# Optimization experiments

Hardware: AMD Instinct MI355X
Metric: run time of the kernel (lower is better)

Reference implementation:

```python
import jax, jax.numpy as jnp
import numpy as np


def _mhc_kernels():
    # Malvar-He-Cutler 5x5 interpolation kernels, shape (4, 1, 5, 5) OIHW
    G_at_RB = np.array([[0, 0, -1, 0, 0], [0, 0, 2, 0, 0], [-1, 2, 4, 2, -1],
                        [0, 0, 2, 0, 0], [0, 0, -1, 0, 0]], dtype=np.float32) / 8
    R_at_G_Rrow = np.array([[0, 0, 0.5, 0, 0], [0, -1, 0, -1, 0], [-1, 4, 5, 4, -1],
                            [0, -1, 0, -1, 0], [0, 0, 0.5, 0, 0]], dtype=np.float32) / 8
    R_at_G_Brow = np.array([[0, 0, -1, 0, 0], [0, -1, 4, -1, 0], [0.5, 0, 5, 0, 0.5],
                            [0, -1, 4, -1, 0], [0, 0, -1, 0, 0]], dtype=np.float32) / 8
    R_at_B = np.array([[0, 0, -1.5, 0, 0], [0, 2, 0, 2, 0], [-1.5, 0, 6, 0, -1.5],
                       [0, 2, 0, 2, 0], [0, 0, -1.5, 0, 0]], dtype=np.float32) / 8
    return np.stack([G_at_RB, R_at_G_Rrow, R_at_G_Brow, R_at_B], axis=0)[:, None, :, :]


def setup_inputs() -> dict:
    key = jax.random.key(0)
    H, W = 4096, 6144  # 24 MP raw frame
    x = jax.random.randint(key, (H, W), 0, 16777216, dtype=jnp.int32)
    kernels = jnp.asarray(_mhc_kernels())  # fixed buffer values, (4,1,5,5)
    return {"x": x, "kernels": kernels}


def reference(x, kernels):
    xf = x.astype(jnp.float32)  # [H, W]
    # reflect pad by 2 and convolve with the 4 MHC kernels in one conv
    xp = jnp.pad(xf, 2, mode="reflect")[None, None]  # [1,1,H+4,W+4]
    res = jax.lax.conv_general_dilated(
        xp, kernels, window_strides=(1, 1), padding="VALID",
        dimension_numbers=("NCHW", "OIHW", "NCHW"))[0]  # [4, H, W]
    Gi, Rgr, Rgb, Rb = res[0], res[1], res[2], res[3]

    z = jnp.zeros_like(xf)
    # RGGB mosaic: R at (even,even), G at (even,odd)+(odd,even), B at (odd,odd)
    R = (z.at[::2, ::2].set(xf[::2, ::2])
           .at[::2, 1::2].set(Rgr[::2, 1::2])
           .at[1::2, ::2].set(Rgb[1::2, ::2])
           .at[1::2, 1::2].set(Rb[1::2, 1::2]))
    G = (z.at[::2, 1::2].set(xf[::2, 1::2])
           .at[1::2, ::2].set(xf[1::2, ::2])
           .at[::2, ::2].set(Gi[::2, ::2])
           .at[1::2, 1::2].set(Gi[1::2, 1::2]))
    B = (z.at[1::2, 1::2].set(xf[1::2, 1::2])
           .at[1::2, ::2].set(Rgr[1::2, ::2])
           .at[::2, 1::2].set(Rgb[::2, 1::2])
           .at[::2, ::2].set(Rb[::2, ::2]))

    rgb = jnp.stack([R, G, B], axis=-1)  # [H, W, 3]
    return jnp.clip(rgb, 0, 16777215).astype(jnp.int32)
```

## Files before the change

### kernel.cpp

```cpp
#include <hip/hip_runtime.h>

#define IMG_H 4096
#define IMG_W 6144

constexpr int TILE_W = 128;
constexpr int TILE_H = 16;
constexpr int LPAD   = 4;
constexpr int PITCH  = 136;
constexpr int LROWS  = 20;

typedef int i4 __attribute__((ext_vector_type(4)));

__device__ __forceinline__ int reflect_h(int r) {
    return r < 0 ? -r : (r >= IMG_H ? 2 * IMG_H - 2 - r : r);
}
__device__ __forceinline__ int reflect_w(int c) {
    return c < 0 ? -c : (c >= IMG_W ? 2 * IMG_W - 2 - c : c);
}
__device__ __forceinline__ int clampi(float v) {
    return (int)fminf(fmaxf(v, 0.f), 16777215.f);
}

__global__ __launch_bounds__(256)
void demosaic_kernel(const int* __restrict__ x, int* __restrict__ out) {
    __shared__ __align__(16) char smem[24576];
    float (*sin_)[PITCH] = (float (*)[PITCH])smem;
    int* sout = (int*)smem;

    const int tid = threadIdx.x;
    const int gx0 = blockIdx.x * TILE_W;
    const int gy0 = blockIdx.y * TILE_H;

    #pragma unroll
    for (int it = 0; it < 3; ++it) {
        int idx = tid + it * 256;
        if (idx < LROWS * 32) {
            int r = idx >> 5, v = idx & 31;
            int gr = reflect_h(gy0 + r - 2);
            i4 q = *(const i4*)(x + (long)gr * IMG_W + gx0 + 4 * v);
            float4 f = make_float4((float)q.x, (float)q.y, (float)q.z, (float)q.w);
            *(float4*)&sin_[r][LPAD + 4 * v] = f;
        }
    }
    if (tid < 80) {
        int r = tid >> 2, h = tid & 3;
        int gr = reflect_h(gy0 + r - 2);
        int lc = (h < 2) ? (2 + h) : (130 + h);
        int gc = reflect_w(gx0 + lc - LPAD);
        sin_[r][lc] = (float)x[(long)gr * IMG_W + gc];
    }
    __syncthreads();

    const int p  = tid & 63;
    const int ty = tid >> 6;
    const int cl = LPAD + 2 * p;

    int rr[4][6];

    #pragma unroll
    for (int k = 0; k < 4; ++k) {
        const int r = ty + 4 * k;
        float w[5][6];
        #pragma unroll
        for (int i = 0; i < 5; ++i) {
            float2 a  = *(const float2*)&sin_[r + i][cl - 2];
            float2 b  = *(const float2*)&sin_[r + i][cl];
            float2 c2 = *(const float2*)&sin_[r + i][cl + 2];
            w[i][0] = a.x;  w[i][1] = a.y;
            w[i][2] = b.x;  w[i][3] = b.y;
            w[i][4] = c2.x; w[i][5] = c2.y;
        }
        const float xe = w[2][2], xo = w[2][3];

        if ((ty & 1) == 0) {
            float Ge = (-w[0][2] + 2.f*(w[1][2]+w[3][2]) + 4.f*w[2][2] - w[4][2]
                        - w[2][0] + 2.f*(w[2][1]+w[2][3]) - w[2][4]) * 0.125f;
            float Ce = (-1.5f*(w[0][2]+w[4][2]+w[2][0]+w[2][4])
                        + 2.f*(w[1][1]+w[1][3]+w[3][1]+w[3][3]) + 6.f*w[2][2]) * 0.125f;
            float RRo = (0.5f*(w[0][3]+w[4][3]) - (w[1][2]+w[1][4]+w[3][2]+w[3][4])
                         - (w[2][1]+w[2][5]) + 4.f*(w[2][2]+w[2][4]) + 5.f*w[2][3]) * 0.125f;
            float RBo = (-(w[0][3]+w[4][3]) - (w[1][2]+w[1][4]+w[3][2]+w[3][4])
                         + 4.f*(w[1][3]+w[3][3]) + 0.5f*(w[2][1]+w[2][5]) + 5.f*w[2][3]) * 0.125f;
            rr[k][0] = clampi(xe);  rr[k][1] = clampi(Ge);  rr[k][2] = clampi(Ce);
            rr[k][3] = clampi(RRo); rr[k][4] = clampi(xo);  rr[k][5] = clampi(RBo);
        } else {
            float RBe = (-(w[0][2]+w[4][2]) - (w[1][1]+w[1][3]+w[3][1]+w[3][3])
                         + 4.f*(w[1][2]+w[3][2]) + 0.5f*(w[2][0]+w[2][4]) + 5.f*w[2][2]) * 0.125f;
            float RRe = (0.5f*(w[0][2]+w[4][2]) - (w[1][1]+w[1][3]+w[3][1]+w[3][3])
                         - (w[2][0]+w[2][4]) + 4.f*(w[2][1]+w[2][3]) + 5.f*w[2][2]) * 0.125f;
            float Co  = (-1.5f*(w[0][3]+w[4][3]+w[2][1]+w[2][5])
                         + 2.f*(w[1][2]+w[1][4]+w[3][2]+w[3][4]) + 6.f*w[2][3]) * 0.125f;
            float Go  = (-w[0][3] + 2.f*(w[1][3]+w[3][3]) + 4.f*w[2][3] - w[4][3]
                         - w[2][1] + 2.f*(w[2][2]+w[2][4]) - w[2][5]) * 0.125f;
            rr[k][0] = clampi(RBe); rr[k][1] = clampi(xe);  rr[k][2] = clampi(RRe);
            rr[k][3] = clampi(Co);  rr[k][4] = clampi(Go);  rr[k][5] = clampi(xo);
        }
    }

    __syncthreads();

    #pragma unroll
    for (int k = 0; k < 4; ++k) {
        int r = ty + 4 * k;
        int2* o = (int2*)&sout[r * (TILE_W * 3) + 6 * p];
        o[0] = make_int2(rr[k][0], rr[k][1]);
        o[1] = make_int2(rr[k][2], rr[k][3]);
        o[2] = make_int2(rr[k][4], rr[k][5]);
    }
    __syncthreads();

    #pragma unroll
    for (int it = 0; it < 6; ++it) {
        int j = tid + it * 256;
        i4 q = *(const i4*)&sout[4 * j];
        int r  = j / 96;
        int wv = j - r * 96;
        int* dst = out + (long)(gy0 + r) * (IMG_W * 3) + gx0 * 3 + 4 * wv;
        __builtin_nontemporal_store(q, (i4*)dst);
    }
}

extern "C" void kernel_launch(void* const* d_in, const int* in_sizes, int n_in,
                              void* d_out, int out_size, void* d_ws, size_t ws_size,
                              hipStream_t stream) {
    const int* x = (const int*)d_in[0];
    int* out = (int*)d_out;
    dim3 grid(IMG_W / TILE_W, IMG_H / TILE_H);
    demosaic_kernel<<<grid, 256, 0, stream>>>(x, out);
}
```

Baseline: 360.2 us.

## Replace LDS tiling with per-wave register sliding window over rows

```diff
diff --git a/kernel.cpp b/kernel.cpp
--- a/kernel.cpp
+++ b/kernel.cpp
@@ -3,76 +3,70 @@
 #define IMG_H 4096
 #define IMG_W 6144
 
-constexpr int TILE_W = 128;
-constexpr int TILE_H = 16;
-constexpr int LPAD   = 4;
-constexpr int PITCH  = 136;
-constexpr int LROWS  = 20;
+constexpr int SH  = 32;
+constexpr int NSX = IMG_W / 128;
+constexpr int NSY = IMG_H / SH;
 
-typedef int i4 __attribute__((ext_vector_type(4)));
+typedef int i2 __attribute__((ext_vector_type(2)));
 
 __device__ __forceinline__ int reflect_h(int r) {
     return r < 0 ? -r : (r >= IMG_H ? 2 * IMG_H - 2 - r : r);
-}
-__device__ __forceinline__ int reflect_w(int c) {
-    return c < 0 ? -c : (c >= IMG_W ? 2 * IMG_W - 2 - c : c);
 }
 __device__ __forceinline__ int clampi(float v) {
     return (int)fminf(fmaxf(v, 0.f), 16777215.f);
 }
 
+struct Row { i2 a, b, c; int fix; };
+
 __global__ __launch_bounds__(256)
-void demosaic_kernel(const int* __restrict__ x, int* __restrict__ out) {
-    __shared__ __align__(16) char smem[24576];
-    float (*sin_)[PITCH] = (float (*)[PITCH])smem;
-    int* sout = (int*)smem;
+void demosaic(const int* __restrict__ x, int* __restrict__ out) {
+    const int wid  = blockIdx.x * 4 + (threadIdx.x >> 6);
+    const int lane = threadIdx.x & 63;
+    const int sx = wid >> 7;
+    const int sy = wid & (NSY - 1);
+    const int gx0 = sx * 128;
+    const int gy0 = sy * SH;
+    const int ce  = gx0 + 2 * lane;
 
-    const int tid = threadIdx.x;
-    const int gx0 = blockIdx.x * TILE_W;
-    const int gy0 = blockIdx.y * TILE_H;
+    const int  cA = max(ce - 2, 0);
+    const int  cB = ce;
+    const int  cC = min(ce + 2, IMG_W - 2);
+    const bool pL = (ce == 0), pR = (ce == IMG_W - 2);
+    const bool pat = pL || pR;
+    const int  fixc = pL ? 2 : IMG_W - 3;
 
-    #pragma unroll
-    for (int it = 0; it < 3; ++it) {
-        int idx = tid + it * 256;
-        if (idx < LROWS * 32) {
-            int r = idx >> 5, v = idx & 31;
-            int gr = reflect_h(gy0 + r - 2);
-            i4 q = *(const i4*)(x + (long)gr * IMG_W + gx0 + 4 * v);
-            float4 f = make_float4((float)q.x, (float)q.y, (float)q.z, (float)q.w);
-            *(float4*)&sin_[r][LPAD + 4 * v] = f;
-        }
+    auto issue = [&](int y, Row& R) {
+        const int* rp = x + (long)reflect_h(y) * IMG_W;
+        R.a = *(const i2*)(rp + cA);
+        R.b = *(const i2*)(rp + cB);
+        R.c = *(const i2*)(rp + cC);
+        if (pat) R.fix = rp[fixc];
+    };
+    auto consume = [&](const Row& R, float* w6) {
+        w6[0] = (float)R.a.x; w6[1] = (float)R.a.y;
+        w6[2] = (float)R.b.x; w6[3] = (float)R.b.y;
+        w6[4] = (float)R.c.x; w6[5] = (float)R.c.y;
+        if (pat) { float f = (float)R.fix; if (pL) w6[0] = f; else w6[5] = f; }
+    };
+
+    float w[5][6];
+    {
+        Row t[4];
+        #pragma unroll
+        for (int i = 0; i < 4; ++i) issue(gy0 - 2 + i, t[i]);
+        #pragma unroll
+        for (int i = 0; i < 4; ++i) consume(t[i], w[i]);
     }
-    if (tid < 80) {
-        int r = tid >> 2, h = tid & 3;
-        int gr = reflect_h(gy0 + r - 2);
-        int lc = (h < 2) ? (2 + h) : (130 + h);
-        int gc = reflect_w(gx0 + lc - LPAD);
-        sin_[r][lc] = (float)x[(long)gr * IMG_W + gc];
-    }
-    __syncthreads();
+    Row pr[2];
+    issue(gy0 + 2, pr[0]);
+    issue(gy0 + 3, pr[1]);
 
-    const int p  = tid & 63;
-    const int ty = tid >> 6;
-    const int cl = LPAD + 2 * p;
+    int* op = out + (long)gy0 * (IMG_W * 3) + ce * 3;
 
-    int rr[4][6];
-
-    #pragma unroll
-    for (int k = 0; k < 4; ++k) {
-        const int r = ty + 4 * k;
-        float w[5][6];
-        #pragma unroll
-        for (int i = 0; i < 5; ++i) {
-            float2 a  = *(const float2*)&sin_[r + i][cl - 2];
-            float2 b  = *(const float2*)&sin_[r + i][cl];
-            float2 c2 = *(const float2*)&sin_[r + i][cl + 2];
-            w[i][0] = a.x;  w[i][1] = a.y;
-            w[i][2] = b.x;  w[i][3] = b.y;
-            w[i][4] = c2.x; w[i][5] = c2.y;
-        }
-        const float xe = w[2][2], xo = w[2][3];
-
-        if ((ty & 1) == 0) {
+    for (int i = 0; i < SH; i += 2) {
+        consume(pr[0], w[4]);
+        if (i < SH - 2) issue(gy0 + i + 4, pr[0]);
+        {
             float Ge = (-w[0][2] + 2.f*(w[1][2]+w[3][2]) + 4.f*w[2][2] - w[4][2]
                         - w[2][0] + 2.f*(w[2][1]+w[2][3]) - w[2][4]) * 0.125f;
             float Ce = (-1.5f*(w[0][2]+w[4][2]+w[2][0]+w[2][4])
@@ -81,9 +75,23 @@
                          - (w[2][1]+w[2][5]) + 4.f*(w[2][2]+w[2][4]) + 5.f*w[2][3]) * 0.125f;
             float RBo = (-(w[0][3]+w[4][3]) - (w[1][2]+w[1][4]+w[3][2]+w[3][4])
                          + 4.f*(w[1][3]+w[3][3]) + 0.5f*(w[2][1]+w[2][5]) + 5.f*w[2][3]) * 0.125f;
-            rr[k][0] = clampi(xe);  rr[k][1] = clampi(Ge);  rr[k][2] = clampi(Ce);
-            rr[k][3] = clampi(RRo); rr[k][4] = clampi(xo);  rr[k][5] = clampi(RBo);
-        } else {
+            i2 q0, q1, q2;
+            q0.x = clampi(w[2][2]); q0.y = clampi(Ge);
+            q1.x = clampi(Ce);      q1.y = clampi(RRo);
+            q2.x = clampi(w[2][3]); q2.y = clampi(RBo);
+            __builtin_nontemporal_store(q0, (i2*)op);
+            __builtin_nontemporal_store(q1, (i2*)(op + 2));
+            __builtin_nontemporal_store(q2, (i2*)(op + 4));
+        }
+        #pragma unroll
+        for (int r = 0; r < 4; ++r)
+            #pragma unroll
+            for (int c = 0; c < 6; ++c) w[r][c] = w[r+1][c];
+        op += IMG_W * 3;
+
+        consume(pr[1], w[4]);
+        if (i < SH - 3) issue(gy0 + i + 5, pr[1]);
+        {
             float RBe = (-(w[0][2]+w[4][2]) - (w[1][1]+w[1][3]+w[3][1]+w[3][3])
                          + 4.f*(w[1][2]+w[3][2]) + 0.5f*(w[2][0]+w[2][4]) + 5.f*w[2][2]) * 0.125f;
             float RRe = (0.5f*(w[0][2]+w[4][2]) - (w[1][1]+w[1][3]+w[3][1]+w[3][3])
@@ -92,31 +100,19 @@
                          + 2.f*(w[1][2]+w[1][4]+w[3][2]+w[3][4]) + 6.f*w[2][3]) * 0.125f;
             float Go  = (-w[0][3] + 2.f*(w[1][3]+w[3][3]) + 4.f*w[2][3] - w[4][3]
                          - w[2][1] + 2.f*(w[2][2]+w[2][4]) - w[2][5]) * 0.125f;
-            rr[k][0] = clampi(RBe); rr[k][1] = clampi(xe);  rr[k][2] = clampi(RRe);
-            rr[k][3] = clampi(Co);  rr[k][4] = clampi(Go);  rr[k][5] = clampi(xo);
+            i2 q0, q1, q2;
+            q0.x = clampi(RBe);     q0.y = clampi(w[2][2]);
+            q1.x = clampi(RRe);     q1.y = clampi(Co);
+            q2.x = clampi(Go);      q2.y = clampi(w[2][3]);
+            __builtin_nontemporal_store(q0, (i2*)op);
+            __builtin_nontemporal_store(q1, (i2*)(op + 2));
+            __builtin_nontemporal_store(q2, (i2*)(op + 4));
         }
-    }
-
-    __syncthreads();
-
-    #pragma unroll
-    for (int k = 0; k < 4; ++k) {
-        int r = ty + 4 * k;
-        int2* o = (int2*)&sout[r * (TILE_W * 3) + 6 * p];
-        o[0] = make_int2(rr[k][0], rr[k][1]);
-        o[1] = make_int2(rr[k][2], rr[k][3]);
-        o[2] = make_int2(rr[k][4], rr[k][5]);
-    }
-    __syncthreads();
-
-    #pragma unroll
-    for (int it = 0; it < 6; ++it) {
-        int j = tid + it * 256;
-        i4 q = *(const i4*)&sout[4 * j];
-        int r  = j / 96;
-        int wv = j - r * 96;
-        int* dst = out + (long)(gy0 + r) * (IMG_W * 3) + gx0 * 3 + 4 * wv;
-        __builtin_nontemporal_store(q, (i4*)dst);
+        #pragma unroll
+        for (int r = 0; r < 4; ++r)
+            #pragma unroll
+            for (int c = 0; c < 6; ++c) w[r][c] = w[r+1][c];
+        op += IMG_W * 3;
     }
 }
 
@@ -125,6 +121,5 @@
                               hipStream_t stream) {
     const int* x = (const int*)d_in[0];
     int* out = (int*)d_out;
-    dim3 grid(IMG_W / TILE_W, IMG_H / TILE_H);
-    demosaic_kernel<<<grid, 256, 0, stream>>>(x, out);
+    demosaic<<<NSX * NSY / 4, 256, 0, stream>>>(x, out);
 }
```

After: 393.7 us. 1.09x slower.
